# Performance work log

Measured on AMD Instinct MI355X. Metric: run time of the kernel, lower is better.

## Reference

```python
import jax, jax.numpy as jnp
import numpy as np

IN_DIM = 256
INNER = IN_DIM // 8  # 32


def setup_inputs() -> dict:
    key = jax.random.key(0)
    ks = jax.random.split(key, 9)
    B, C, W, H = 4, IN_DIM, 64, 64
    sc = 0.05
    return {
        "x": jax.random.normal(ks[0], (B, C, W, H), dtype=jnp.float32),
        "Wf": jax.random.normal(ks[1], (INNER, C), dtype=jnp.float32) * sc,
        "bf": jnp.zeros((INNER,), dtype=jnp.float32),
        "Wg": jax.random.normal(ks[2], (INNER, C), dtype=jnp.float32) * sc,
        "bg": jnp.zeros((INNER,), dtype=jnp.float32),
        "Wh": jax.random.normal(ks[3], (INNER, C), dtype=jnp.float32) * sc,
        "bh": jnp.zeros((INNER,), dtype=jnp.float32),
        "Wv": jax.random.normal(ks[4], (C, INNER), dtype=jnp.float32) * sc,
        "bv": jnp.zeros((C,), dtype=jnp.float32),
        "gamma": jnp.ones((1,), dtype=jnp.float32) * 0.5,  # nonzero so attention path matters
    }


def reference(x, Wf, bf, Wg, bg, Wh, bh, Wv, bv, gamma):
    B, C, W, H = x.shape
    N = W * H
    xf = x.reshape(B, C, N)
    # 1x1 convs == per-pixel linear projections
    f = jnp.einsum('kc,bcn->bkn', Wf, xf) + bf[None, :, None]  # [B, C/8, N]
    g = jnp.einsum('kc,bcn->bkn', Wg, xf) + bg[None, :, None]
    h = jnp.einsum('kc,bcn->bkn', Wh, xf) + bh[None, :, None]
    # s[b,n,m] = sum_k f[b,k,n] * g[b,k,m]  (f^T @ g)
    s = jnp.einsum('bkn,bkm->bnm', f, g)                      # [B, N, N]
    attn = jax.nn.softmax(s, axis=-1)                          # softmax over last dim
    attn_map = jnp.transpose(attn, (0, 2, 1))                  # returned map (permuted)
    # o_pre = h_x @ attn_map : o_pre[b,k,m] = sum_n h[b,k,n] * attn[b,m,n]
    o_pre = jnp.einsum('bkn,bmn->bkm', h, attn)                # [B, C/8, N]
    o = jnp.einsum('ck,bkn->bcn', Wv, o_pre) + bv[None, :, None]
    o = o.reshape(B, C, W, H)
    y = gamma.reshape(()) * o + x
    return (y, attn_map)
```

## Files before the change

kernel.cpp:

```cpp
#include <hip/hip_runtime.h>
#include <cstddef>
#include <cstdint>

#define NB     4
#define CDIM   256
#define KD     32
#define NPIX   4096
#define SSHIFT 20.0f

typedef __attribute__((ext_vector_type(8))) short  bfrag;
typedef __attribute__((ext_vector_type(4))) float  facc;

#define MFMA(a,b,c) __builtin_amdgcn_mfma_f32_16x16x32_bf16((a),(b),(c),0,0,0)

__device__ __forceinline__ unsigned short f2bf(float x) {
    union { float f; unsigned u; } v; v.f = x;
    unsigned u = v.u + 0x7fffu + ((v.u >> 16) & 1u);
    return (unsigned short)(u >> 16);
}
__device__ __forceinline__ float bf2f(unsigned short h) {
    union { float f; unsigned u; } v; v.u = ((unsigned)h) << 16;
    return v.f;
}

#define OFF_FA_HI (0)
#define OFF_FA_LO (1u<<20)
#define OFF_GB_HI (2u<<20)
#define OFF_GB_LO (3u<<20)
#define OFF_HB    (4u<<20)
#define OFF_WA_HI (5u<<20)
#define OFF_WA_LO ((5u<<20) + 65536)
#define OFF_OT    ((5u<<20) + 131072)
#define OFF_RCP   ((5u<<20) + 131072 + (2u<<20))

__global__ __launch_bounds__(256) void wt_kernel(const float* __restrict__ Wf,
                                                 const float* __restrict__ Wg,
                                                 const float* __restrict__ Wh,
                                                 unsigned short* __restrict__ WA_hi,
                                                 unsigned short* __restrict__ WA_lo)
{
    int t = blockIdx.x * 256 + threadIdx.x;
    if (t >= 48 * 64) return;
    int tile = t >> 6, lane = t & 63;
    int rt = tile >> 3, cc = tile & 7;
    int q = lane >> 4, c15 = lane & 15;
    int row = rt * 16 + c15;
    const float* W = (row < 32) ? (Wf + (size_t)row * CDIM)
                   : (row < 64) ? (Wg + (size_t)(row - 32) * CDIM)
                                : (Wh + (size_t)(row - 64) * CDIM);
    int cb = cc * 32 + q * 8;
    bfrag vh, vl;
#pragma unroll
    for (int j = 0; j < 8; ++j) {
        float xv = W[cb + j];
        unsigned short h = f2bf(xv);
        vh[j] = (short)h;
        vl[j] = (short)f2bf(xv - bf2f(h));
    }
    *(bfrag*)(WA_hi + (size_t)t * 8) = vh;
    *(bfrag*)(WA_lo + (size_t)t * 8) = vl;
}

__global__ __launch_bounds__(256) void proj_kernel(const float* __restrict__ x,
                                                   const unsigned short* __restrict__ WA_hi,
                                                   const unsigned short* __restrict__ WA_lo,
                                                   const float* __restrict__ bfv,
                                                   const float* __restrict__ bgv,
                                                   const float* __restrict__ bhv,
                                                   unsigned short* __restrict__ fA_hi,
                                                   unsigned short* __restrict__ fA_lo,
                                                   unsigned short* __restrict__ gB_hi,
                                                   unsigned short* __restrict__ gB_lo,
                                                   unsigned short* __restrict__ hB)
{
    __shared__ float xs[32][65];
    __shared__ float os[96][65];
    __shared__ float bias_s[96];

    const int b  = blockIdx.y;
    const int n0 = blockIdx.x * 64;
    const int tid = threadIdx.x;
    const int w = tid >> 6, lane = tid & 63, q = lane >> 4, c15 = lane & 15;

    if (tid < 96)
        bias_s[tid] = (tid < 32) ? bfv[tid] : (tid < 64 ? bgv[tid - 32] : bhv[tid - 64]);

    facc acc[6];
#pragma unroll
    for (int rt = 0; rt < 6; ++rt) acc[rt] = (facc){0.f, 0.f, 0.f, 0.f};

    const float* xb = x + (size_t)b * CDIM * NPIX + n0;
    const int cr = tid >> 3, nb = (tid & 7) * 8;

    for (int cc = 0; cc < 8; ++cc) {
        const float* src = xb + (size_t)(cc * 32 + cr) * NPIX + nb;
        float4 va = *(const float4*)src;
        float4 vb = *(const float4*)(src + 4);
        __syncthreads();
        *(float4*)&xs[cr][nb]     = va;
        *(float4*)&xs[cr][nb + 4] = vb;
        __syncthreads();

        bfrag xh, xl;
#pragma unroll
        for (int j = 0; j < 8; ++j) {
            float xv = xs[q * 8 + j][w * 16 + c15];
            unsigned short h = f2bf(xv);
            xh[j] = (short)h;
            xl[j] = (short)f2bf(xv - bf2f(h));
        }
#pragma unroll
        for (int rt = 0; rt < 6; ++rt) {
            size_t wo = ((size_t)(rt * 8 + cc) * 64 + lane) * 8;
            bfrag wh = *(const bfrag*)(WA_hi + wo);
            bfrag wl = *(const bfrag*)(WA_lo + wo);
            acc[rt] = MFMA(wh, xh, acc[rt]);
            acc[rt] = MFMA(wh, xl, acc[rt]);
            acc[rt] = MFMA(wl, xh, acc[rt]);
        }
    }

#pragma unroll
    for (int rt = 0; rt < 6; ++rt)
#pragma unroll
        for (int i = 0; i < 4; ++i) {
            int row = rt * 16 + q * 4 + i;
            os[row][w * 16 + c15] = acc[rt][i] + bias_s[row];
        }
    __syncthreads();

    {
        bfrag vh, vl;
#pragma unroll
        for (int j = 0; j < 8; ++j) {
            float v = os[q * 8 + j][w * 16 + c15];
            unsigned short h = f2bf(v);
            vh[j] = (short)h; vl[j] = (short)f2bf(v - bf2f(h));
        }
        size_t o = ((size_t)(b * 256 + (n0 >> 4) + w) * 64 + lane) * 8;
        *(bfrag*)(fA_hi + o) = vh;
        *(bfrag*)(fA_lo + o) = vl;
#pragma unroll
        for (int j = 0; j < 8; ++j) {
            float v = os[32 + q * 8 + j][w * 16 + c15];
            unsigned short h = f2bf(v);
            vh[j] = (short)h; vl[j] = (short)f2bf(v - bf2f(h));
        }
        *(bfrag*)(gB_hi + o) = vh;
        *(bfrag*)(gB_lo + o) = vl;
        int mcl = w >> 1, kt = w & 1;
        bfrag hv;
#pragma unroll
        for (int j = 0; j < 8; ++j) {
            int p = q * 8 + j;
            int mp = (p & 1) * 16 + (p >> 1);
            float v = os[64 + kt * 16 + c15][mcl * 32 + mp];
            hv[j] = (short)f2bf(v);
        }
        size_t oh = ((size_t)((b * 128 + (n0 >> 5) + mcl) * 2 + kt) * 64 + lane) * 8;
        *(bfrag*)(hB + oh) = hv;
    }
}

#define ATTN1_STEP(G0H,G1H,G0L,G1L,H0,H1)                                       \
    {                                                                           \
        facc s0 = (facc){0.f,0.f,0.f,0.f}, s1 = (facc){0.f,0.f,0.f,0.f};        \
        s0 = MFMA(fh, G0H, s0); s0 = MFMA(fh, G0L, s0); s0 = MFMA(fl, G0H, s0); \
        s1 = MFMA(fh, G1H, s1); s1 = MFMA(fh, G1L, s1); s1 = MFMA(fl, G1H, s1); \
        float e0[4], e1[4];                                                     \
        _Pragma("unroll")                                                       \
        for (int i = 0; i < 4; ++i) {                                           \
            e0[i] = __expf(s0[i] - SSHIFT);                                     \
            e1[i] = __expf(s1[i] - SSHIFT);                                     \
            sum[i] += e0[i] + e1[i];                                            \
        }                                                                       \
        _Pragma("unroll")                                                       \
        for (int i = 0; i < 4; ++i) {                                           \
            unsigned pr = (unsigned)f2bf(e0[i]) | ((unsigned)f2bf(e1[i]) << 16);\
            *(unsigned*)&P[(4 * q + i) * 40 + 2 * c15] = pr;                    \
        }                                                                       \
        bfrag pA = *(const bfrag*)&P[c15 * 40 + q * 8];                         \
        o0 = MFMA(pA, H0, o0);                                                  \
        o1 = MFMA(pA, H1, o1);                                                  \
    }

__global__ __launch_bounds__(256) void attn_kernel(const unsigned short* __restrict__ fA_hi,
                                                   const unsigned short* __restrict__ fA_lo,
                                                   const unsigned short* __restrict__ gB_hi,
                                                   const unsigned short* __restrict__ gB_lo,
                                                   const unsigned short* __restrict__ hB,
                                                   float* __restrict__ rcp_g,
                                                   float* __restrict__ oT)
{
    __shared__ unsigned short Pst[4][16 * 40];
    __shared__ float red[4][64][8];
    __shared__ float sums_l[4][16];
    __shared__ float rcp_l[16];

    const int bid = blockIdx.x;
    const int xcd = bid & 7, jj = bid >> 3;
    const int b  = xcd >> 1;
    const int r0 = ((xcd & 1) * 128 + jj) * 16;
    const int tid = threadIdx.x;
    const int w = tid >> 6, lane = tid & 63, q = lane >> 4, c15 = lane & 15;

    const size_t fo = ((size_t)(b * 256 + (r0 >> 4)) * 64 + lane) * 8;
    const bfrag fh = *(const bfrag*)(fA_hi + fo);
    const bfrag fl = *(const bfrag*)(fA_lo + fo);

    facc o0 = (facc){0.f,0.f,0.f,0.f}, o1 = (facc){0.f,0.f,0.f,0.f};
    float sum[4] = {0.f, 0.f, 0.f, 0.f};
    unsigned short* P = &Pst[w][0];

    const int ch0 = w * 32, ch1 = ch0 + 32;

    size_t go = ((size_t)(b * 256 + 2 * ch0) * 64 + lane) * 8;
    size_t ho = ((size_t)((b * 128 + ch0) * 2) * 64 + lane) * 8;
    bfrag g0h = *(const bfrag*)(gB_hi + go);
    bfrag g1h = *(const bfrag*)(gB_hi + go + 512);
    bfrag g0l = *(const bfrag*)(gB_lo + go);
    bfrag g1l = *(const bfrag*)(gB_lo + go + 512);
    bfrag h0  = *(const bfrag*)(hB + ho);
    bfrag h1  = *(const bfrag*)(hB + ho + 512);

    for (int mc = ch0; mc < ch1 - 1; ++mc) {
        go += 1024; ho += 1024;
        bfrag ng0h = *(const bfrag*)(gB_hi + go);
        bfrag ng1h = *(const bfrag*)(gB_hi + go + 512);
        bfrag ng0l = *(const bfrag*)(gB_lo + go);
        bfrag ng1l = *(const bfrag*)(gB_lo + go + 512);
        bfrag nh0  = *(const bfrag*)(hB + ho);
        bfrag nh1  = *(const bfrag*)(hB + ho + 512);
        ATTN1_STEP(g0h, g1h, g0l, g1l, h0, h1);
        g0h = ng0h; g1h = ng1h; g0l = ng0l; g1l = ng1l; h0 = nh0; h1 = nh1;
    }
    ATTN1_STEP(g0h, g1h, g0l, g1l, h0, h1);

#pragma unroll
    for (int m = 1; m < 16; m <<= 1)
#pragma unroll
        for (int i = 0; i < 4; ++i) sum[i] += __shfl_xor(sum[i], m);
    if (c15 == 0) {
#pragma unroll
        for (int i = 0; i < 4; ++i) sums_l[w][4 * q + i] = sum[i];
    }
    *(facc*)&red[w][lane][0] = o0;
    *(facc*)&red[w][lane][4] = o1;
    __syncthreads();
    if (tid < 16) {
        float rv = 1.0f / (sums_l[0][tid] + sums_l[1][tid] + sums_l[2][tid] + sums_l[3][tid]);
        rcp_l[tid] = rv;
        rcp_g[(size_t)b * NPIX + r0 + tid] = rv;
    }
    __syncthreads();

    if (w == 0) {
        facc a = (facc){0.f,0.f,0.f,0.f}, bb = (facc){0.f,0.f,0.f,0.f};
#pragma unroll
        for (int ww = 0; ww < 4; ++ww) {
            a  += *(const facc*)&red[ww][lane][0];
            bb += *(const facc*)&red[ww][lane][4];
        }
#pragma unroll
        for (int i = 0; i < 4; ++i) {
            int r = 4 * q + i;
            float rc = rcp_l[r];
            oT[((size_t)(b * NPIX + r0 + r)) * KD + c15]      = a[i] * rc;
            oT[((size_t)(b * NPIX + r0 + r)) * KD + 16 + c15] = bb[i] * rc;
        }
    }
}

#define ATTN2_STEP(BH,BL,RC,N)                                                  \
    {                                                                           \
        facc s = (facc){0.f,0.f,0.f,0.f};                                       \
        s = MFMA(a_hi, BH, s);                                                  \
        s = MFMA(a_hi, BL, s);                                                  \
        s = MFMA(a_lo, BH, s);                                                  \
        _Pragma("unroll")                                                       \
        for (int i = 0; i < 4; ++i)                                             \
            amrow[(size_t)i * NPIX + (N)] = __expf(s[i] - SSHIFT) * (RC);       \
    }

__global__ __launch_bounds__(256) void attn2_kernel(const unsigned short* __restrict__ fA_hi,
                                                    const unsigned short* __restrict__ fA_lo,
                                                    const unsigned short* __restrict__ gB_hi,
                                                    const unsigned short* __restrict__ gB_lo,
                                                    const float* __restrict__ rcp_g,
                                                    float* __restrict__ am)
{
    const int bid = blockIdx.x;
    const int xcd = bid & 7, jj = bid >> 3;
    const int b  = xcd >> 1;
    const int mt = (xcd & 1) * 128 + jj;
    const int tid = threadIdx.x;
    const int w = tid >> 6, lane = tid & 63, q = lane >> 4, c15 = lane & 15;

    const size_t ga = ((size_t)(b * 256 + mt) * 64 + lane) * 8;
    const bfrag a_hi = *(const bfrag*)(gB_hi + ga);
    const bfrag a_lo = *(const bfrag*)(gB_lo + ga);

    const int m0 = mt * 16 + q * 4;
    float* amrow = am + (size_t)b * NPIX * NPIX + (size_t)m0 * NPIX;
    const float* rcp_b = rcp_g + (size_t)b * NPIX;

    size_t fo = ((size_t)(b * 256 + w * 64) * 64 + lane) * 8;
    int n = (w * 64) * 16 + c15;
    bfrag bh = *(const bfrag*)(fA_hi + fo);
    bfrag bl = *(const bfrag*)(fA_lo + fo);
    float rc = rcp_b[n];

    for (int t = 0; t < 63; ++t) {
        fo += 512;
        bfrag nbh = *(const bfrag*)(fA_hi + fo);
        bfrag nbl = *(const bfrag*)(fA_lo + fo);
        float nrc = rcp_b[n + 16];
        ATTN2_STEP(bh, bl, rc, n);
        bh = nbh; bl = nbl; rc = nrc; n += 16;
    }
    ATTN2_STEP(bh, bl, rc, n);
}

__global__ __launch_bounds__(256) void out_kernel(const float* __restrict__ x,
                                                  const float* __restrict__ oT,
                                                  const float* __restrict__ Wv,
                                                  const float* __restrict__ bv,
                                                  const float* __restrict__ gamma,
                                                  float* __restrict__ y)
{
    __shared__ float wv_s[CDIM * KD];
    const int b  = blockIdx.y;
    const int tid = threadIdx.x;
    const int n = blockIdx.x * 64 + (tid & 63);
    const int cg = tid >> 6;

    for (int i = tid * 4; i < CDIM * KD; i += 1024)
        *(float4*)&wv_s[i] = *(const float4*)&Wv[i];

    float op[KD];
    {
        const float4* src = (const float4*)&oT[((size_t)(b * NPIX + n)) * KD];
#pragma unroll
        for (int qq = 0; qq < 8; ++qq) {
            float4 v = src[qq];
            op[qq * 4 + 0] = v.x; op[qq * 4 + 1] = v.y;
            op[qq * 4 + 2] = v.z; op[qq * 4 + 3] = v.w;
        }
    }
    __syncthreads();
    const float gm = gamma[0];

    for (int c = cg * 64; c < cg * 64 + 64; ++c) {
        float a = 0.f;
#pragma unroll
        for (int k4 = 0; k4 < 8; ++k4) {
            float4 wv4 = *(const float4*)&wv_s[c * KD + k4 * 4];
            a = fmaf(wv4.x, op[k4 * 4 + 0], a);
            a = fmaf(wv4.y, op[k4 * 4 + 1], a);
            a = fmaf(wv4.z, op[k4 * 4 + 2], a);
            a = fmaf(wv4.w, op[k4 * 4 + 3], a);
        }
        size_t idx = ((size_t)(b * CDIM + c)) * NPIX + n;
        y[idx] = fmaf(gm, a + bv[c], x[idx]);
    }
}

extern "C" void kernel_launch(void* const* d_in, const int* in_sizes, int n_in,
                              void* d_out, int out_size, void* d_ws, size_t ws_size,
                              hipStream_t stream)
{
    const float* x     = (const float*)d_in[0];
    const float* Wf    = (const float*)d_in[1];
    const float* bfv   = (const float*)d_in[2];
    const float* Wg    = (const float*)d_in[3];
    const float* bgv   = (const float*)d_in[4];
    const float* Wh    = (const float*)d_in[5];
    const float* bhv   = (const float*)d_in[6];
    const float* Wv    = (const float*)d_in[7];
    const float* bv    = (const float*)d_in[8];
    const float* gamma = (const float*)d_in[9];

    char* ws = (char*)d_ws;
    unsigned short* fA_hi = (unsigned short*)(ws + OFF_FA_HI);
    unsigned short* fA_lo = (unsigned short*)(ws + OFF_FA_LO);
    unsigned short* gB_hi = (unsigned short*)(ws + OFF_GB_HI);
    unsigned short* gB_lo = (unsigned short*)(ws + OFF_GB_LO);
    unsigned short* hB    = (unsigned short*)(ws + OFF_HB);
    unsigned short* WA_hi = (unsigned short*)(ws + OFF_WA_HI);
    unsigned short* WA_lo = (unsigned short*)(ws + OFF_WA_LO);
    float*          oT    = (float*)(ws + OFF_OT);
    float*          rcp_g = (float*)(ws + OFF_RCP);

    float* y  = (float*)d_out;
    float* am = (float*)d_out + (size_t)NB * CDIM * NPIX;

    hipLaunchKernelGGL(wt_kernel, dim3(12), dim3(256), 0, stream, Wf, Wg, Wh, WA_hi, WA_lo);
    hipLaunchKernelGGL(proj_kernel, dim3(NPIX / 64, NB), dim3(256), 0, stream,
                       x, WA_hi, WA_lo, bfv, bgv, bhv, fA_hi, fA_lo, gB_hi, gB_lo, hB);
    hipLaunchKernelGGL(attn_kernel, dim3(1024), dim3(256), 0, stream,
                       fA_hi, fA_lo, gB_hi, gB_lo, hB, rcp_g, oT);
    hipLaunchKernelGGL(attn2_kernel, dim3(1024), dim3(256), 0, stream,
                       fA_hi, fA_lo, gB_hi, gB_lo, rcp_g, am);
    hipLaunchKernelGGL(out_kernel, dim3(NPIX / 64, NB), dim3(256), 0, stream,
                       x, oT, Wv, bv, gamma, y);
}
```

Measured before the change: 424.8 us.

## Retile attention-map kernel to two row tiles per block with nontemporal stores

The attention-map writer kernel now has each block compute two 16-row m-tiles over half of the n range. This reuses each loaded f fragment across two MFMA chains. The 256 MB map write and the y write use nontemporal stores to avoid polluting cache. The block-to-XCD mapping changes, and the loop is partially unrolled with an occupancy hint, which may alter write locality and register pressure.

```diff
diff --git a/kernel.cpp b/kernel.cpp
--- a/kernel.cpp
+++ b/kernel.cpp
@@ -273,44 +273,53 @@
 
 #define ATTN2_STEP(BH,BL,RC,N)                                                  \
     {                                                                           \
-        facc s = (facc){0.f,0.f,0.f,0.f};                                       \
-        s = MFMA(a_hi, BH, s);                                                  \
-        s = MFMA(a_hi, BL, s);                                                  \
-        s = MFMA(a_lo, BH, s);                                                  \
+        facc s0 = (facc){0.f,0.f,0.f,0.f}, s1 = (facc){0.f,0.f,0.f,0.f};        \
+        s0 = MFMA(a0h, BH, s0); s0 = MFMA(a0h, BL, s0); s0 = MFMA(a0l, BH, s0); \
+        s1 = MFMA(a1h, BH, s1); s1 = MFMA(a1h, BL, s1); s1 = MFMA(a1l, BH, s1); \
         _Pragma("unroll")                                                       \
-        for (int i = 0; i < 4; ++i)                                             \
-            amrow[(size_t)i * NPIX + (N)] = __expf(s[i] - SSHIFT) * (RC);       \
-    }
-
-__global__ __launch_bounds__(256) void attn2_kernel(const unsigned short* __restrict__ fA_hi,
-                                                    const unsigned short* __restrict__ fA_lo,
-                                                    const unsigned short* __restrict__ gB_hi,
-                                                    const unsigned short* __restrict__ gB_lo,
-                                                    const float* __restrict__ rcp_g,
-                                                    float* __restrict__ am)
+        for (int i = 0; i < 4; ++i) {                                           \
+            __builtin_nontemporal_store(__expf(s0[i] - SSHIFT) * (RC),          \
+                                        &amrow0[(size_t)i * NPIX + (N)]);       \
+            __builtin_nontemporal_store(__expf(s1[i] - SSHIFT) * (RC),          \
+                                        &amrow1[(size_t)i * NPIX + (N)]);       \
+        }                                                                       \
+    }
+
+__global__ __launch_bounds__(256, 4) void attn2_kernel(const unsigned short* __restrict__ fA_hi,
+                                                       const unsigned short* __restrict__ fA_lo,
+                                                       const unsigned short* __restrict__ gB_hi,
+                                                       const unsigned short* __restrict__ gB_lo,
+                                                       const float* __restrict__ rcp_g,
+                                                       float* __restrict__ am)
 {
     const int bid = blockIdx.x;
-    const int xcd = bid & 7, jj = bid >> 3;
-    const int b  = xcd >> 1;
-    const int mt = (xcd & 1) * 128 + jj;
+    const int nh = bid & 1;
+    const int mp = (bid >> 1) & 127;
+    const int b  = bid >> 8;
     const int tid = threadIdx.x;
     const int w = tid >> 6, lane = tid & 63, q = lane >> 4, c15 = lane & 15;
 
-    const size_t ga = ((size_t)(b * 256 + mt) * 64 + lane) * 8;
-    const bfrag a_hi = *(const bfrag*)(gB_hi + ga);
-    const bfrag a_lo = *(const bfrag*)(gB_lo + ga);
-
-    const int m0 = mt * 16 + q * 4;
-    float* amrow = am + (size_t)b * NPIX * NPIX + (size_t)m0 * NPIX;
+    const size_t ga = ((size_t)(b * 256 + 2 * mp) * 64 + lane) * 8;
+    const bfrag a0h = *(const bfrag*)(gB_hi + ga);
+    const bfrag a0l = *(const bfrag*)(gB_lo + ga);
+    const bfrag a1h = *(const bfrag*)(gB_hi + ga + 512);
+    const bfrag a1l = *(const bfrag*)(gB_lo + ga + 512);
+
+    const int m0 = mp * 32 + q * 4;
+    float* amrow0 = am + (size_t)b * NPIX * NPIX + (size_t)m0 * NPIX;
+    float* amrow1 = amrow0 + (size_t)16 * NPIX;
     const float* rcp_b = rcp_g + (size_t)b * NPIX;
 
-    size_t fo = ((size_t)(b * 256 + w * 64) * 64 + lane) * 8;
-    int n = (w * 64) * 16 + c15;
+    const int nt0 = nh * 128 + w * 32;
+    size_t fo = ((size_t)(b * 256 + nt0) * 64 + lane) * 8;
+    int n = nt0 * 16 + c15;
+
     bfrag bh = *(const bfrag*)(fA_hi + fo);
     bfrag bl = *(const bfrag*)(fA_lo + fo);
     float rc = rcp_b[n];
 
-    for (int t = 0; t < 63; ++t) {
+#pragma unroll 4
+    for (int t = 0; t < 31; ++t) {
         fo += 512;
         bfrag nbh = *(const bfrag*)(fA_hi + fo);
         bfrag nbl = *(const bfrag*)(fA_lo + fo);
@@ -361,7 +370,7 @@
             a = fmaf(wv4.w, op[k4 * 4 + 3], a);
         }
         size_t idx = ((size_t)(b * CDIM + c)) * NPIX + n;
-        y[idx] = fmaf(gm, a + bv[c], x[idx]);
+        __builtin_nontemporal_store(fmaf(gm, a + bv[c], x[idx]), &y[idx]);
     }
 }
 
```

New measurement: 417.2 us. About the same (-1.8%).
